# Kernel optimization log

Hardware: AMD Instinct MI355X
Metric: run time of the kernel (lower is better)

## Reference

```python
import jax, jax.numpy as jnp
import numpy as np

DICE_TH = 0.4
CLS_TH = 0.5
LN_EPS = 1e-5


def setup_inputs() -> dict:
    key = jax.random.key(0)
    P, C, NC, K = 200_000, 256, 200, 24  # points, clicks, classes, latent prototypes
    ks = jax.random.split(key, 6)
    # structured masks: each click targets one of K prototype regions so the
    # dice/cls thresholds yield a non-degenerate grouping
    point_proto = jax.random.randint(ks[0], (P,), 0, K)
    proto_vals = jax.random.uniform(ks[1], (P,))
    click_proto = jax.random.randint(ks[2], (C,), 0, K)
    base = (point_proto[:, None] == click_proto[None, :]).astype(jnp.float32)  # [P, C]
    noise = jax.random.uniform(ks[3], (P, C))
    masks_heatmap = base * (0.6 + 0.4 * proto_vals[:, None]) + 0.02 * noise
    class_emb = jax.random.normal(ks[4], (K, NC)) * 3.0
    cls_logits = class_emb[click_proto] + 0.3 * jax.random.normal(ks[5], (C, NC))
    clicks_list = jax.random.randint(ks[0], (C,), 0, NC)  # unused (random_clicks=True)
    return {"masks_heatmap": masks_heatmap, "cls_logits": cls_logits,
            "clicks_list": clicks_list}


def _associate(masks_heatmap, cls_logits):
    """Greedy dice+cls-similarity grouping (random_clicks=True path).
    Returns labels[c] = leader click index of the group containing click c."""
    M = masks_heatmap                      # [P, C]
    C = M.shape[1]
    s = M.sum(0)                           # [C]
    # dice[i, j] = 2 * m_i . m_j / (sum(m_i) + sum(m_j))  (all pairs at once)
    dice = 2.0 * (M.T @ M) / (s[:, None] + s[None, :])
    # F.layer_norm over last dim, no affine
    mu = cls_logits.mean(-1, keepdims=True)
    var = ((cls_logits - mu) ** 2).mean(-1, keepdims=True)
    p = (cls_logits - mu) / jnp.sqrt(var + LN_EPS)
    sim = p @ p.T                          # [C, C]
    cond = (dice > DICE_TH) & (sim > CLS_TH)

    def step(carry, x):
        assigned, labels = carry
        i, row = x
        # skip if i already suppressed; take unsuppressed clicks matching row i
        take = row & (~assigned) & (~assigned[i])
        return (assigned | take, jnp.where(take, i, labels)), None

    init = (jnp.zeros((C,), bool), jnp.full((C,), -1, jnp.int32))
    (assigned, labels), _ = jax.lax.scan(
        step, init, (jnp.arange(C, dtype=jnp.int32), cond))
    return labels


def _merge(labels, masks_heatmap, cls_logits):
    """reduction='max': per-group max over member clicks. Unused group slots
    (non-leader indices) are zero-filled and flagged by group_valid."""
    C = masks_heatmap.shape[1]
    seg = jnp.where(labels >= 0, labels, C)  # route unassigned to dump segment
    counts = jax.ops.segment_sum(jnp.ones((C,), jnp.float32), seg,
                                 num_segments=C + 1)[:C]
    group_valid = counts > 0
    nm = jax.ops.segment_max(masks_heatmap.T, seg, num_segments=C + 1)[:C]  # [C, P]
    nc = jax.ops.segment_max(cls_logits, seg, num_segments=C + 1)[:C]      # [C, NC]
    new_masks = jnp.where(group_valid[:, None], nm, 0.0).T  # [P, C]
    new_cls = jnp.where(group_valid[:, None], nc, 0.0)      # [C, NC]
    return new_masks, new_cls, group_valid


def reference(masks_heatmap, cls_logits, clicks_list):
    labels = _associate(masks_heatmap, cls_logits)
    new_masks, new_cls, group_valid = _merge(labels, masks_heatmap, cls_logits)
    return labels, group_valid, new_masks, new_cls
```

## Files before the change

kernel.cpp:

```cpp
#include <hip/hip_runtime.h>
#include <cstdint>
#include <cstddef>

constexpr int P  = 200000;
constexpr int C  = 256;
constexpr int NC = 200;
#define DICE_TH 0.4f
#define CLS_TH  0.5f
#define LN_EPS  1e-5f

constexpr int KC = 800;
constexpr int NCHUNK = 250;
constexpr int NSTEP = KC / 32;

constexpr size_t WS_G       = 0;
constexpr size_t WS_S       = 262144;
constexpr size_t WS_PROW    = 263168;
constexpr size_t WS_PT      = 467968;
constexpr size_t WS_COND    = 672768;
constexpr size_t WS_MSTART  = 680960;
constexpr size_t WS_MEMBERS = 682240;

typedef float floatx16 __attribute__((ext_vector_type(16)));
typedef __bf16 bf16x8 __attribute__((ext_vector_type(8)));
typedef unsigned short ushort8 __attribute__((ext_vector_type(8)));

__device__ __forceinline__ unsigned short f2bf(float f) {
  unsigned u = __builtin_bit_cast(unsigned, f);
  unsigned r = u + 0x7FFFu + ((u >> 16) & 1u);
  return (unsigned short)(r >> 16);
}

constexpr int LDA = 40;

__global__ __launch_bounds__(256, 2) void gram_mfma_kernel(
    const float* __restrict__ M, float* __restrict__ G, float* __restrict__ s) {
  __shared__ unsigned short Abf[128 * LDA];
  __shared__ unsigned short Bbf[128 * LDA];

  const int type = blockIdx.x;
  const int i0 = (type == 2) ? 128 : 0;
  const int j0 = (type == 0) ? 0 : 128;
  const bool diag = (type != 1);
  const int tid = threadIdx.x;
  const int wv = tid >> 6, lane = tid & 63;
  const int c = tid & 127, h = tid >> 7;
  const int k0 = blockIdx.y * KC;

  floatx16 acc[4];
#pragma unroll
  for (int t = 0; t < 4; ++t)
#pragma unroll
    for (int r = 0; r < 16; ++r) acc[t][r] = 0.f;
  float ssum = 0.f;

  const int mrow = lane & 31;
  const int kgrp = (lane >> 5) * 8;

  float va[16], vb[16];
  {
    const float* colA = M + (size_t)(k0 + h * 16) * 256 + i0 + c;
#pragma unroll
    for (int u = 0; u < 16; ++u) va[u] = colA[(size_t)u * 256];
    if (!diag) {
      const float* colB = M + (size_t)(k0 + h * 16) * 256 + j0 + c;
#pragma unroll
      for (int u = 0; u < 16; ++u) vb[u] = colB[(size_t)u * 256];
    }
  }

  for (int step = 0; step < NSTEP; ++step) {
    {
      if (diag) {
#pragma unroll
        for (int u = 0; u < 16; ++u) ssum += va[u];
      }
      ushort8 lo, hi;
#pragma unroll
      for (int u = 0; u < 8; ++u) { lo[u] = f2bf(va[u]); hi[u] = f2bf(va[u + 8]); }
      *reinterpret_cast<ushort8*>(&Abf[c * LDA + h * 16]) = lo;
      *reinterpret_cast<ushort8*>(&Abf[c * LDA + h * 16 + 8]) = hi;
      if (!diag) {
#pragma unroll
        for (int u = 0; u < 8; ++u) { lo[u] = f2bf(vb[u]); hi[u] = f2bf(vb[u + 8]); }
        *reinterpret_cast<ushort8*>(&Bbf[c * LDA + h * 16]) = lo;
        *reinterpret_cast<ushort8*>(&Bbf[c * LDA + h * 16 + 8]) = hi;
      }
    }
    __syncthreads();

    if (step + 1 < NSTEP) {
      const int kb = k0 + (step + 1) * 32 + h * 16;
      const float* colA = M + (size_t)kb * 256 + i0 + c;
#pragma unroll
      for (int u = 0; u < 16; ++u) va[u] = colA[(size_t)u * 256];
      if (!diag) {
        const float* colB = M + (size_t)kb * 256 + j0 + c;
#pragma unroll
        for (int u = 0; u < 16; ++u) vb[u] = colB[(size_t)u * 256];
      }
    }

    const unsigned short* Bsrc = diag ? Abf : Bbf;
#pragma unroll
    for (int sub = 0; sub < 2; ++sub) {
      const int ko = sub * 16 + kgrp;
      bf16x8 a = __builtin_bit_cast(
          bf16x8, *reinterpret_cast<const ushort8*>(
                      &Abf[(32 * wv + mrow) * LDA + ko]));
#pragma unroll
      for (int t = 0; t < 4; ++t) {
        bf16x8 b = __builtin_bit_cast(
            bf16x8, *reinterpret_cast<const ushort8*>(
                        &Bsrc[(32 * t + mrow) * LDA + ko]));
        acc[t] = __builtin_amdgcn_mfma_f32_32x32x16_bf16(a, b, acc[t], 0, 0, 0);
      }
    }
    __syncthreads();
  }

#pragma unroll
  for (int t = 0; t < 4; ++t) {
    const int gc = j0 + 32 * t + (lane & 31);
#pragma unroll
    for (int r = 0; r < 16; ++r) {
      const int gr = i0 + 32 * wv + (r & 3) + 8 * (r >> 2) + 4 * (lane >> 5);
      atomicAdd(&G[(size_t)gr * 256 + gc], acc[t][r]);
    }
  }
  if (diag) atomicAdd(&s[i0 + c], ssum);
}

__global__ __launch_bounds__(64) void ln_kernel(const float* __restrict__ cls,
                                                float* __restrict__ p_row,
                                                float* __restrict__ pT) {
  const int c = blockIdx.x;
  const int t = threadIdx.x;
  const float* x = cls + (size_t)c * NC;
  float v0 = x[t];
  float v1 = x[t + 64];
  float v2 = (t < 72) ? x[t + 128] : 0.f;

  float sum = v0 + v1 + v2;
#pragma unroll
  for (int o = 32; o > 0; o >>= 1) sum += __shfl_xor(sum, o);
  const float mu = sum / (float)NC;

  float d0 = v0 - mu, d1 = v1 - mu, d2 = (t < 72) ? (v2 - mu) : 0.f;
  float sq = d0 * d0 + d1 * d1 + d2 * d2;
#pragma unroll
  for (int o = 32; o > 0; o >>= 1) sq += __shfl_xor(sq, o);
  const float var = sq / (float)NC;
  const float inv = 1.0f / sqrtf(var + LN_EPS);

  float p0 = d0 * inv, p1 = d1 * inv, p2 = d2 * inv;
  p_row[(size_t)c * NC + t] = p0;
  p_row[(size_t)c * NC + t + 64] = p1;
  pT[(size_t)t * C + c] = p0;
  pT[(size_t)(t + 64) * C + c] = p1;
  if (t < 72) {
    p_row[(size_t)c * NC + t + 128] = p2;
    pT[(size_t)(t + 128) * C + c] = p2;
  }
}

__global__ __launch_bounds__(256) void cond_kernel(
    const float* __restrict__ G, const float* __restrict__ s,
    const float* __restrict__ p_row, const float* __restrict__ pT,
    unsigned long long* __restrict__ condW) {
  __shared__ float pi[NC];
  const int i = blockIdx.x;
  const int j = threadIdx.x;
  if (j < NC) pi[j] = p_row[(size_t)i * NC + j];
  __syncthreads();

  const float si = s[i];
  const float sj = s[j];
  const float g = (i >= 128 && j < 128) ? G[(size_t)j * C + i]
                                        : G[(size_t)i * C + j];
  const float dice = 2.f * g / (si + sj);

  float a0 = 0.f, a1 = 0.f, a2 = 0.f, a3 = 0.f;
#pragma unroll 2
  for (int k = 0; k < NC; k += 4) {
    a0 = fmaf(pi[k + 0], pT[(size_t)(k + 0) * C + j], a0);
    a1 = fmaf(pi[k + 1], pT[(size_t)(k + 1) * C + j], a1);
    a2 = fmaf(pi[k + 2], pT[(size_t)(k + 2) * C + j], a2);
    a3 = fmaf(pi[k + 3], pT[(size_t)(k + 3) * C + j], a3);
  }
  const float acc = (a0 + a1) + (a2 + a3);

  const bool cnd = (dice > DICE_TH) && (acc > CLS_TH);
  unsigned long long m = __ballot(cnd);
  if ((j & 63) == 0) condW[i * 4 + (j >> 6)] = m;
}

__global__ __launch_bounds__(64) void scan_kernel(
    const unsigned long long* __restrict__ condW,
    float* __restrict__ out_labels, float* __restrict__ out_valid,
    int* __restrict__ mstart, int* __restrict__ members) {
  __shared__ unsigned long long cS[C * 4];
  __shared__ int cnt[C];
  __shared__ int ms[C + 1];
  const int t = threadIdx.x;

  for (int idx = t; idx < C * 4; idx += 64) cS[idx] = condW[idx];
  for (int idx = t; idx < C; idx += 64) cnt[idx] = 0;
  __syncthreads();

  unsigned long long asg[4] = {0ull, 0ull, 0ull, 0ull};
  int lab[4] = {-1, -1, -1, -1};

  unsigned long long r0 = cS[0], r1 = cS[1], r2 = cS[2], r3 = cS[3];
  for (int i = 0; i < C; ++i) {
    const int nx = (i + 1 < C) ? (i + 1) * 4 : 0;
    unsigned long long n0 = cS[nx], n1 = cS[nx + 1], n2 = cS[nx + 2],
                       n3 = cS[nx + 3];
    const int w = i >> 6, b = i & 63;
    if (!((asg[w] >> b) & 1ull)) {
      unsigned long long tk;
      tk = r0 & ~asg[0]; asg[0] |= tk; if ((tk >> t) & 1ull) lab[0] = i;
      tk = r1 & ~asg[1]; asg[1] |= tk; if ((tk >> t) & 1ull) lab[1] = i;
      tk = r2 & ~asg[2]; asg[2] |= tk; if ((tk >> t) & 1ull) lab[2] = i;
      tk = r3 & ~asg[3]; asg[3] |= tk; if ((tk >> t) & 1ull) lab[3] = i;
    }
    r0 = n0; r1 = n1; r2 = n2; r3 = n3;
  }

#pragma unroll
  for (int w = 0; w < 4; ++w)
    if (lab[w] >= 0) atomicAdd(&cnt[lab[w]], 1);
  __syncthreads();

  if (t == 0) {
    ms[0] = 0;
    for (int c2 = 0; c2 < C; ++c2) ms[c2 + 1] = ms[c2] + cnt[c2];
  }
  __syncthreads();
  for (int idx = t; idx < C; idx += 64) cnt[idx] = ms[idx];
  __syncthreads();
#pragma unroll
  for (int w = 0; w < 4; ++w) {
    if (lab[w] >= 0) {
      int pos = atomicAdd(&cnt[lab[w]], 1);
      members[pos] = w * 64 + t;
    }
  }
#pragma unroll
  for (int w = 0; w < 4; ++w) {
    const int col = w * 64 + t;
    out_labels[col] = (float)lab[w];
    out_valid[col] = (ms[col + 1] > ms[col]) ? 1.0f : 0.0f;
  }
  for (int idx = t; idx < C + 1; idx += 64) mstart[idx] = ms[idx];
}

__global__ __launch_bounds__(256) void merge_masks_kernel(
    const float* __restrict__ M, const int* __restrict__ mstart,
    const int* __restrict__ members, float* __restrict__ out_masks) {
  __shared__ float rows[16 * 256];
  __shared__ int msS[C + 1];
  __shared__ int memS[C];
  const int tid = threadIdx.x;
  const size_t p0 = (size_t)blockIdx.x * 16;

  msS[tid] = mstart[tid];
  if (tid == 0) msS[C] = mstart[C];
  memS[tid] = members[tid];

  const float4* src = reinterpret_cast<const float4*>(M + p0 * 256);
#pragma unroll
  for (int it = 0; it < 4; ++it)
    reinterpret_cast<float4*>(rows)[it * 256 + tid] = src[it * 256 + tid];
  __syncthreads();

  const int st = msS[tid], en = msS[tid + 1];
  float mx[16];
  if (en > st) {
    const int m0 = memS[st];
#pragma unroll
    for (int r = 0; r < 16; ++r) mx[r] = rows[r * 256 + m0];
    for (int k = st + 1; k < en; ++k) {
      const int mm = memS[k];
#pragma unroll
      for (int r = 0; r < 16; ++r) mx[r] = fmaxf(mx[r], rows[r * 256 + mm]);
    }
  } else {
#pragma unroll
    for (int r = 0; r < 16; ++r) mx[r] = 0.f;
  }
#pragma unroll
  for (int r = 0; r < 16; ++r) out_masks[(p0 + r) * 256 + tid] = mx[r];
}

__global__ __launch_bounds__(256) void merge_cls_kernel(
    const float* __restrict__ cls, const int* __restrict__ mstart,
    const int* __restrict__ members, float* __restrict__ out_cls) {
  __shared__ int se[2];
  const int c = blockIdx.x;
  const int t = threadIdx.x;
  if (t < 2) se[t] = mstart[c + t];
  __syncthreads();
  const int st = se[0], en = se[1];
  if (t < NC) {
    float mx = 0.f;
    if (en > st) {
      mx = cls[(size_t)members[st] * NC + t];
      for (int k = st + 1; k < en; ++k)
        mx = fmaxf(mx, cls[(size_t)members[k] * NC + t]);
    }
    out_cls[(size_t)c * NC + t] = mx;
  }
}

extern "C" void kernel_launch(void* const* d_in, const int* in_sizes, int n_in,
                              void* d_out, int out_size, void* d_ws,
                              size_t ws_size, hipStream_t stream) {
  const float* M = (const float*)d_in[0];
  const float* cls = (const float*)d_in[1];

  float* out = (float*)d_out;
  char* ws = (char*)d_ws;
  float* G = (float*)(ws + WS_G);
  float* s = (float*)(ws + WS_S);
  float* p_row = (float*)(ws + WS_PROW);
  float* pT = (float*)(ws + WS_PT);
  unsigned long long* condW = (unsigned long long*)(ws + WS_COND);
  int* mstart = (int*)(ws + WS_MSTART);
  int* members = (int*)(ws + WS_MEMBERS);

  float* out_labels = out;
  float* out_valid = out + 256;
  float* out_masks = out + 512;
  float* out_cls = out + 512 + (size_t)P * 256;

  hipMemsetAsync(ws, 0, WS_S + 1024, stream);

  gram_mfma_kernel<<<dim3(3, NCHUNK), 256, 0, stream>>>(M, G, s);
  ln_kernel<<<C, 64, 0, stream>>>(cls, p_row, pT);
  cond_kernel<<<C, 256, 0, stream>>>(G, s, p_row, pT, condW);
  scan_kernel<<<1, 64, 0, stream>>>(condW, out_labels, out_valid, mstart,
                                    members);
  merge_masks_kernel<<<P / 16, 256, 0, stream>>>(M, mstart, members, out_masks);
  merge_cls_kernel<<<C, 256, 0, stream>>>(cls, mstart, members, out_cls);
}
```

Before: 464.1 us.

## Replace Gram atomics with per-chunk partial buffers and a separate reduction kernel

The Gram kernel no longer atomically adds each accumulator element into the shared 256x256 G matrix. Each K-chunk block now writes its MFMA fragments with vectorized float4 stores into a private partial buffer (about 49 MB of workspace). A new reduce kernel sums the 250 partials, remaps fragment order to matrix coordinates and mirrors the off-diagonal tile, which simplifies the indexing in cond_kernel. This removes atomic contention and the memset of G, at the cost of extra global traffic (write plus read of ~49 MB) and one more launch; the launch bound's occupancy hint also rises from 2 to 3.

```diff
diff --git a/kernel.cpp b/kernel.cpp
--- a/kernel.cpp
+++ b/kernel.cpp
@@ -12,14 +12,16 @@
 constexpr int KC = 800;
 constexpr int NCHUNK = 250;
 constexpr int NSTEP = KC / 32;
-
-constexpr size_t WS_G       = 0;
-constexpr size_t WS_S       = 262144;
-constexpr size_t WS_PROW    = 263168;
-constexpr size_t WS_PT      = 467968;
-constexpr size_t WS_COND    = 672768;
-constexpr size_t WS_MSTART  = 680960;
-constexpr size_t WS_MEMBERS = 682240;
+constexpr int GP_CHUNK = 3 * 16384;
+
+constexpr size_t WS_GP      = 0;
+constexpr size_t WS_G       = 49152000;
+constexpr size_t WS_S       = WS_G + 262144;
+constexpr size_t WS_PROW    = WS_S + 1024;
+constexpr size_t WS_PT      = WS_PROW + 204800;
+constexpr size_t WS_COND    = WS_PT + 204800;
+constexpr size_t WS_MSTART  = WS_COND + 8192;
+constexpr size_t WS_MEMBERS = WS_MSTART + 1280;
 
 typedef float floatx16 __attribute__((ext_vector_type(16)));
 typedef __bf16 bf16x8 __attribute__((ext_vector_type(8)));
@@ -33,8 +35,9 @@
 
 constexpr int LDA = 40;
 
-__global__ __launch_bounds__(256, 2) void gram_mfma_kernel(
-    const float* __restrict__ M, float* __restrict__ G, float* __restrict__ s) {
+__global__ __launch_bounds__(256, 3) void gram_mfma_kernel(
+    const float* __restrict__ M, float* __restrict__ Gp,
+    float* __restrict__ s) {
   __shared__ unsigned short Abf[128 * LDA];
   __shared__ unsigned short Bbf[128 * LDA];
 
@@ -119,16 +122,52 @@
     __syncthreads();
   }
 
+  float* base = Gp + (size_t)blockIdx.y * GP_CHUNK + type * 16384;
 #pragma unroll
   for (int t = 0; t < 4; ++t) {
-    const int gc = j0 + 32 * t + (lane & 31);
-#pragma unroll
-    for (int r = 0; r < 16; ++r) {
-      const int gr = i0 + 32 * wv + (r & 3) + 8 * (r >> 2) + 4 * (lane >> 5);
-      atomicAdd(&G[(size_t)gr * 256 + gc], acc[t][r]);
+    float* dst = base + (((wv * 4 + t) * 64 + lane) * 16);
+#pragma unroll
+    for (int q = 0; q < 4; ++q) {
+      float4 v = make_float4(acc[t][4 * q], acc[t][4 * q + 1],
+                             acc[t][4 * q + 2], acc[t][4 * q + 3]);
+      *reinterpret_cast<float4*>(dst + 4 * q) = v;
     }
   }
   if (diag) atomicAdd(&s[i0 + c], ssum);
+}
+
+__global__ __launch_bounds__(256) void reduce_g_kernel(
+    const float* __restrict__ Gp, float* __restrict__ G) {
+  const int e = blockIdx.x * 256 + threadIdx.x;
+  const float* p = Gp + e;
+  float s0 = 0.f, s1 = 0.f, s2 = 0.f, s3 = 0.f, s4 = 0.f;
+  float s5 = 0.f, s6 = 0.f, s7 = 0.f, s8 = 0.f, s9 = 0.f;
+  for (int ch = 0; ch < NCHUNK; ch += 10) {
+    s0 += p[(size_t)(ch + 0) * GP_CHUNK];
+    s1 += p[(size_t)(ch + 1) * GP_CHUNK];
+    s2 += p[(size_t)(ch + 2) * GP_CHUNK];
+    s3 += p[(size_t)(ch + 3) * GP_CHUNK];
+    s4 += p[(size_t)(ch + 4) * GP_CHUNK];
+    s5 += p[(size_t)(ch + 5) * GP_CHUNK];
+    s6 += p[(size_t)(ch + 6) * GP_CHUNK];
+    s7 += p[(size_t)(ch + 7) * GP_CHUNK];
+    s8 += p[(size_t)(ch + 8) * GP_CHUNK];
+    s9 += p[(size_t)(ch + 9) * GP_CHUNK];
+  }
+  const float sum = (((s0 + s1) + (s2 + s3)) + ((s4 + s5) + (s6 + s7))) +
+                    (s8 + s9);
+
+  const int tile = e >> 14;
+  const int r = e & 15;
+  const int lane = (e >> 4) & 63;
+  const int wvt = (e >> 10) & 15;
+  const int wv = wvt >> 2, tt = wvt & 3;
+  const int i0 = (tile == 2) ? 128 : 0;
+  const int j0 = (tile == 0) ? 0 : 128;
+  const int gr = i0 + 32 * wv + (r & 3) + 8 * (r >> 2) + 4 * (lane >> 5);
+  const int gc = j0 + 32 * tt + (lane & 31);
+  G[(size_t)gr * 256 + gc] = sum;
+  if (tile == 1) G[(size_t)gc * 256 + gr] = sum;
 }
 
 __global__ __launch_bounds__(64) void ln_kernel(const float* __restrict__ cls,
@@ -176,8 +215,7 @@
 
   const float si = s[i];
   const float sj = s[j];
-  const float g = (i >= 128 && j < 128) ? G[(size_t)j * C + i]
-                                        : G[(size_t)i * C + j];
+  const float g = G[(size_t)i * C + j];
   const float dice = 2.f * g / (si + sj);
 
   float a0 = 0.f, a1 = 0.f, a2 = 0.f, a3 = 0.f;
@@ -321,6 +359,7 @@
 
   float* out = (float*)d_out;
   char* ws = (char*)d_ws;
+  float* Gp = (float*)(ws + WS_GP);
   float* G = (float*)(ws + WS_G);
   float* s = (float*)(ws + WS_S);
   float* p_row = (float*)(ws + WS_PROW);
@@ -334,9 +373,10 @@
   float* out_masks = out + 512;
   float* out_cls = out + 512 + (size_t)P * 256;
 
-  hipMemsetAsync(ws, 0, WS_S + 1024, stream);
-
-  gram_mfma_kernel<<<dim3(3, NCHUNK), 256, 0, stream>>>(M, G, s);
+  hipMemsetAsync(ws + WS_S, 0, 1024, stream);
+
+  gram_mfma_kernel<<<dim3(3, NCHUNK), 256, 0, stream>>>(M, Gp, s);
+  reduce_g_kernel<<<GP_CHUNK / 256, 256, 0, stream>>>(Gp, G);
   ln_kernel<<<C, 64, 0, stream>>>(cls, p_row, pT);
   cond_kernel<<<C, 256, 0, stream>>>(G, s, p_row, pT, condW);
   scan_kernel<<<1, 64, 0, stream>>>(condW, out_labels, out_valid, mstart,
```

New measurement: 472.4 us. Within noise of the previous version (+1.8%).
